# Kernel tuning notes

Measured on AMD Instinct MI355X. Metric: run time of the kernel, lower is better.

The kernel has to match this reference:

```python
import jax, jax.numpy as jnp
import numpy as np

BSZ = 2          # batch
H_IMG = 180      # BEV height
W_IMG = 180      # BEV width
BLK = 15         # block_size
D = 128          # d_model
NH = 8           # nhead
DH = D // NH     # head dim


def _bn_relu(x, g, b, m, v, eps=1e-5):
    # eval-mode BatchNorm2d followed by ReLU; x is NCHW
    s = g * jax.lax.rsqrt(v + eps)
    return jax.nn.relu((x - m[None, :, None, None]) * s[None, :, None, None]
                       + b[None, :, None, None])


def _split_tokens(x):
    # (B,C,H,W) -> (B*nb, blk*blk, C), block order = (row-block, col-block)
    B, C, H, W = x.shape
    hb, wb = H // BLK, W // BLK
    x = x.reshape(B, C, hb, BLK, wb, BLK)
    x = x.transpose(0, 2, 4, 1, 3, 5)              # (B,hb,wb,C,blk,blk)
    x = x.reshape(B * hb * wb, C, BLK * BLK)
    return x.transpose(0, 2, 1)                    # (B*nb, L, C)


def _merge_tokens(t, B, H, W):
    # (B*nb, L, C) -> (B,C,H,W), inverse of _split_tokens
    hb, wb = H // BLK, W // BLK
    C = t.shape[-1]
    x = t.transpose(0, 2, 1).reshape(B, hb, wb, C, BLK, BLK)
    x = x.transpose(0, 3, 1, 4, 2, 5)              # (B,C,hb,blk,wb,blk)
    return x.reshape(B, C, H, W)


def setup_inputs() -> dict:
    key = jax.random.key(0)
    ks = jax.random.split(key, 16)
    n = lambda i, shp, sc=0.05: jax.random.normal(ks[i], shp, jnp.float32) * sc
    inp = {
        'camera_feat': jax.random.normal(ks[0], (BSZ, 80, H_IMG, W_IMG), jnp.float32),
        'lidar_feat': jax.random.normal(ks[1], (BSZ, 256, H_IMG, W_IMG), jnp.float32),
        'cam_w': n(2, (D, 80)),
        'cam_gamma': jnp.ones((D,), jnp.float32),
        'cam_beta': jnp.zeros((D,), jnp.float32),
        'cam_mean': n(3, (D,)),
        'cam_var': jax.random.uniform(ks[4], (D,), jnp.float32, 0.5, 1.5),
        'lidar_w': n(5, (D, 256)),
        'lidar_gamma': jnp.ones((D,), jnp.float32),
        'lidar_beta': jnp.zeros((D,), jnp.float32),
        'lidar_mean': n(6, (D,)),
        'lidar_var': jax.random.uniform(ks[7], (D,), jnp.float32, 0.5, 1.5),
        'in_proj_w': n(8, (3 * D, D)),
        'in_proj_b': jnp.zeros((3 * D,), jnp.float32),
        'out_proj_w': n(9, (D, D)),
        'out_proj_b': jnp.zeros((D,), jnp.float32),
        'outc_w': n(10, (256, D, 3, 3)),
        'outc_gamma': jnp.ones((256,), jnp.float32),
        'outc_beta': jnp.zeros((256,), jnp.float32),
        'outc_mean': n(11, (256,)),
        'outc_var': jax.random.uniform(ks[12], (256,), jnp.float32, 0.5, 1.5),
    }
    return inp


def reference(camera_feat, lidar_feat,
              cam_w, cam_gamma, cam_beta, cam_mean, cam_var,
              lidar_w, lidar_gamma, lidar_beta, lidar_mean, lidar_var,
              in_proj_w, in_proj_b, out_proj_w, out_proj_b,
              outc_w, outc_gamma, outc_beta, outc_mean, outc_var):
    B, _, H, W = camera_feat.shape
    # 1x1 conv projections + BN + ReLU
    cam_p = _bn_relu(jnp.einsum('bchw,dc->bdhw', camera_feat, cam_w),
                     cam_gamma, cam_beta, cam_mean, cam_var)
    lid_p = _bn_relu(jnp.einsum('bchw,dc->bdhw', lidar_feat, lidar_w),
                     lidar_gamma, lidar_beta, lidar_mean, lidar_var)
    # windowed tokens: (B*nb, L=225, D)
    cam_t = _split_tokens(cam_p)
    lid_t = _split_tokens(lid_p)
    # cross-attention: query=lidar, key/value=camera (torch MHA math)
    wq, wk, wv = in_proj_w[:D], in_proj_w[D:2 * D], in_proj_w[2 * D:]
    bq, bk, bv = in_proj_b[:D], in_proj_b[D:2 * D], in_proj_b[2 * D:]
    BN, L, _ = lid_t.shape
    q = (lid_t @ wq.T + bq).reshape(BN, L, NH, DH).transpose(0, 2, 1, 3)
    k = (cam_t @ wk.T + bk).reshape(BN, L, NH, DH).transpose(0, 2, 1, 3)
    v = (cam_t @ wv.T + bv).reshape(BN, L, NH, DH).transpose(0, 2, 1, 3)
    scores = jnp.einsum('bhqd,bhkd->bhqk', q, k) / jnp.sqrt(jnp.float32(DH))
    attn = jax.nn.softmax(scores, axis=-1)
    ctx = jnp.einsum('bhqk,bhkd->bhqd', attn, v)
    ctx = ctx.transpose(0, 2, 1, 3).reshape(BN, L, D)
    attn_out = ctx @ out_proj_w.T + out_proj_b
    # merge windows back and fuse
    fused = _merge_tokens(attn_out, B, H, W) + lid_p
    # 3x3 conv + BN + ReLU
    y = jax.lax.conv_general_dilated(
        fused, outc_w, window_strides=(1, 1), padding='SAME',
        dimension_numbers=('NCHW', 'OIHW', 'NCHW'))
    return _bn_relu(y, outc_gamma, outc_beta, outc_mean, outc_var)
```

## Files before the change

### kernel.cpp

```cpp
#include <hip/hip_runtime.h>
#include <hip/hip_bf16.h>
#include <cmath>

#define HW      32400
#define WIMG    180
#define DD      128
#define NHEADS  8
#define DHEAD   16
#define LTOK    225
#define PSTRIDE 64928
#define FBROW   188
#define FBH     182
#define FBSZ    ((size_t)FBH * FBROW * 128)

typedef __attribute__((ext_vector_type(8))) short bf16x8;
typedef __attribute__((ext_vector_type(4))) float f32x4;

union U16B { uint4 u; int4 i; bf16x8 v; };

__device__ __forceinline__ bf16x8 ldfrag(const __hip_bfloat16* p, int ld, int lane) {
  return *(const bf16x8*)(p + (size_t)(lane & 15) * ld + ((lane >> 4) << 3));
}

__device__ __forceinline__ float bf2f(unsigned int u) {
  return __uint_as_float(u << 16);
}

__device__ __forceinline__ unsigned short f2bf(float x) {
  unsigned int b = __float_as_uint(x);
  return (unsigned short)((b + 0x7fffu + ((b >> 16) & 1u)) >> 16);
}

__global__ void k_cast(const float* __restrict__ in, __hip_bfloat16* __restrict__ out, int n) {
  int i = blockIdx.x * 256 + threadIdx.x;
  if (i < n) out[i] = __float2bfloat16(in[i]);
}

__global__ void k_prepproj(const float* __restrict__ w, __hip_bfloat16* __restrict__ wb,
                           int C, int Kpad) {
  int i = blockIdx.x * 256 + threadIdx.x;
  if (i >= 128 * Kpad) return;
  int d = i / Kpad, c = i % Kpad;
  wb[i] = (c < C) ? __float2bfloat16(w[d * C + c]) : __float2bfloat16(0.f);
}

__global__ void k_prepw2(const float* __restrict__ cw, __hip_bfloat16* __restrict__ wcb) {
  int i = blockIdx.x * 256 + threadIdx.x;
  if (i >= 294912) return;
  int oc16  = i / 18432;
  int r0    = i % 18432;
  int tap   = r0 / 2048;
  int r1    = r0 % 2048;
  int chunk = r1 / 512;
  int r2    = r1 % 512;
  int lane  = r2 / 8;
  int e     = r2 % 8;
  int oc = oc16 * 16 + (lane & 15);
  int ic = chunk * 32 + (lane >> 4) * 8 + e;
  wcb[i] = __float2bfloat16(cw[(size_t)(oc * 128 + ic) * 9 + tap]);
}

__global__ void k_zero(uint4* __restrict__ p, int n16) {
  int i = blockIdx.x * 256 + threadIdx.x;
  if (i < n16) p[i] = make_uint4(0u, 0u, 0u, 0u);
}

__global__ void __launch_bounds__(256) k_proj_mfma(
    const float* __restrict__ in, const __hip_bfloat16* __restrict__ wb,
    const float* __restrict__ g, const float* __restrict__ be,
    const float* __restrict__ mu, const float* __restrict__ var,
    __hip_bfloat16* __restrict__ outp, int C, int Kpad) {
  __shared__ __align__(16) __hip_bfloat16 sa[128 * 64];
  int m0 = blockIdx.x * 128;
  int b = blockIdx.z;
  int tid = threadIdx.x, lane = tid & 63, wid = tid >> 6;
  int wm = (wid >> 1) * 64, wn = (wid & 1) * 64;
  const float* inb = in + (size_t)b * C * HW;
  int sp = (tid >> 1) & 127;
  int sc4 = (tid & 1) * 4;
  int gp = m0 + sp;
  bool pok = gp < HW;
  f32x4 acc[4][4] = {};
  for (int kc = 0; kc < Kpad; kc += 64) {
    __syncthreads();
#pragma unroll
    for (int it = 0; it < 8; ++it) {
      int lc = sc4 + it * 8;
      int c = kc + lc;
      unsigned short u[4];
#pragma unroll
      for (int j = 0; j < 4; ++j) {
        float x = (pok && (c + j) < C) ? inb[(size_t)(c + j) * HW + gp] : 0.f;
        u[j] = f2bf(x);
      }
      int blk = (lc >> 3) ^ (sp & 7);
      char* dst = (char*)sa + sp * 128 + blk * 16 + (lc & 7) * 2;
      *(uint2*)dst = make_uint2(((unsigned)u[1] << 16) | u[0],
                                ((unsigned)u[3] << 16) | u[2]);
    }
    __syncthreads();
#pragma unroll
    for (int ks = 0; ks < 2; ++ks) {
      bf16x8 af[4], bfr[4];
#pragma unroll
      for (int i = 0; i < 4; ++i) {
        int pr = wm + i * 16 + (lane & 15);
        int blk = ((ks * 4 + (lane >> 4)) ^ (pr & 7));
        af[i] = *(const bf16x8*)((const char*)sa + pr * 128 + blk * 16);
      }
#pragma unroll
      for (int j = 0; j < 4; ++j)
        bfr[j] = ldfrag(wb + (size_t)(wn + j * 16) * Kpad + kc + ks * 32, Kpad, lane);
#pragma unroll
      for (int i = 0; i < 4; ++i)
#pragma unroll
        for (int j = 0; j < 4; ++j)
          acc[i][j] = __builtin_amdgcn_mfma_f32_16x16x32_bf16(af[i], bfr[j], acc[i][j], 0, 0, 0);
    }
  }
  int col = lane & 15, rq = lane >> 4;
  __hip_bfloat16* ob = outp + (size_t)b * PSTRIDE * 128;
#pragma unroll
  for (int j = 0; j < 4; ++j) {
    int d = wn + j * 16 + col;
    float s = g[d] * rsqrtf(var[d] + 1e-5f);
    float mm = mu[d], bb = be[d];
#pragma unroll
    for (int i = 0; i < 4; ++i) {
#pragma unroll
      for (int r = 0; r < 4; ++r) {
        int m = m0 + wm + i * 16 + rq * 4 + r;
        if (m < HW) {
          float y = (acc[i][j][r] - mm) * s + bb;
          ob[(size_t)m * 128 + d] = __float2bfloat16(fmaxf(y, 0.f));
        }
      }
    }
  }
}

__global__ void __launch_bounds__(256) k_gemm_bias(
    const __hip_bfloat16* __restrict__ A, const __hip_bfloat16* __restrict__ B,
    const float* __restrict__ bias, __hip_bfloat16* __restrict__ out,
    int K, int ldout) {
  int m0 = blockIdx.x * 128, n0 = blockIdx.y * 128, b = blockIdx.z;
  int lane = threadIdx.x & 63, wid = threadIdx.x >> 6;
  int wm = (wid >> 1) * 64, wn = (wid & 1) * 64;
  const __hip_bfloat16* Ab = A + (size_t)b * PSTRIDE * K;
  f32x4 acc[4][4] = {};
  for (int kc = 0; kc < K; kc += 32) {
    bf16x8 af[4], bfr[4];
#pragma unroll
    for (int i = 0; i < 4; ++i)
      af[i] = ldfrag(Ab + (size_t)(m0 + wm + i * 16) * K + kc, K, lane);
#pragma unroll
    for (int j = 0; j < 4; ++j)
      bfr[j] = ldfrag(B + (size_t)(n0 + wn + j * 16) * K + kc, K, lane);
#pragma unroll
    for (int i = 0; i < 4; ++i)
#pragma unroll
      for (int j = 0; j < 4; ++j)
        acc[i][j] = __builtin_amdgcn_mfma_f32_16x16x32_bf16(af[i], bfr[j], acc[i][j], 0, 0, 0);
  }
  int col = lane & 15, rq = lane >> 4;
  __hip_bfloat16* ob = out + (size_t)b * PSTRIDE * ldout;
#pragma unroll
  for (int j = 0; j < 4; ++j) {
    int n = n0 + wn + j * 16 + col;
    float bs = bias[n];
#pragma unroll
    for (int i = 0; i < 4; ++i) {
#pragma unroll
      for (int r = 0; r < 4; ++r) {
        int m = m0 + wm + i * 16 + rq * 4 + r;
        if (m < HW) ob[(size_t)m * ldout + n] = __float2bfloat16(acc[i][j][r] + bs);
      }
    }
  }
}

__global__ void __launch_bounds__(256) k_attn_mfma(
    const __hip_bfloat16* __restrict__ qc, const __hip_bfloat16* __restrict__ kvb,
    __hip_bfloat16* __restrict__ ctx) {
  __shared__ __align__(16) unsigned short ksh[240 * 32];
  __shared__ __align__(16) unsigned short vsh[16 * 248];
  __shared__ __align__(16) unsigned short psh[4 * 256];
  int bn = blockIdx.x, hh = blockIdx.y;
  int b = bn / 144, rr = bn % 144, tby = rr / 12, tbx = rr % 12;
  int tid = threadIdx.x;
  int pbase = tby * 15 * WIMG + tbx * 15;
  const __hip_bfloat16* kvbase = kvb + (size_t)b * PSTRIDE * 256 + hh * 16;

  if (tid < 240) {
    int row = tid;
    unsigned short kv16[16];
#pragma unroll
    for (int j = 0; j < 16; ++j) kv16[j] = 0;
    unsigned short vv16[16];
#pragma unroll
    for (int j = 0; j < 16; ++j) vv16[j] = 0;
    if (row < LTOK) {
      int p = pbase + (row / 15) * WIMG + (row % 15);
      const uint4* kp = (const uint4*)(kvbase + (size_t)p * 256);
      uint4 k0 = kp[0], k1 = kp[1];
      uint4 v0 = kp[16], v1 = kp[17];
      unsigned kw[8] = {k0.x, k0.y, k0.z, k0.w, k1.x, k1.y, k1.z, k1.w};
      unsigned vw[8] = {v0.x, v0.y, v0.z, v0.w, v1.x, v1.y, v1.z, v1.w};
#pragma unroll
      for (int j = 0; j < 8; ++j) {
        kv16[2 * j]     = (unsigned short)(__float_as_uint(bf2f(kw[j] & 0xffffu) * 0.25f) >> 16);
        kv16[2 * j + 1] = (unsigned short)(__float_as_uint(bf2f(kw[j] >> 16) * 0.25f) >> 16);
        vv16[2 * j]     = (unsigned short)(vw[j] & 0xffffu);
        vv16[2 * j + 1] = (unsigned short)(vw[j] >> 16);
      }
    }
    char* kbase = (char*)ksh + row * 64;
    uint4 zz = make_uint4(0, 0, 0, 0);
    *(uint4*)(kbase + ((0 ^ (row & 3)) << 4)) = ((uint4*)kv16)[0];
    *(uint4*)(kbase + ((1 ^ (row & 3)) << 4)) = ((uint4*)kv16)[1];
    *(uint4*)(kbase + ((2 ^ (row & 3)) << 4)) = zz;
    *(uint4*)(kbase + ((3 ^ (row & 3)) << 4)) = zz;
#pragma unroll
    for (int d = 0; d < 16; ++d) vsh[d * 248 + row] = vv16[d];
  }
  __syncthreads();

  int lane = tid & 63, wid = tid >> 6;
  int g = lane >> 4, q15 = lane & 15;
  int wq0 = wid * 64;
  char* pw_base = (char*)psh + wid * 512;

  bf16x8 qf[4];
#pragma unroll
  for (int i = 0; i < 4; ++i) {
    int q = wq0 + i * 16 + q15;
    int qq = q < LTOK ? q : 0;
    int p = pbase + (qq / 15) * WIMG + (qq % 15);
    U16B u; u.u = make_uint4(0, 0, 0, 0);
    if (g < 2) u.u = *(const uint4*)(qc + ((size_t)b * PSTRIDE + p) * 128 + hh * 16 + g * 8);
    qf[i] = u.v;
  }

  float m_[4], ls[4];
  f32x4 oac[4] = {};
#pragma unroll
  for (int i = 0; i < 4; ++i) { m_[i] = -3.0e38f; ls[i] = 0.f; }
  const f32x4 zacc = {};

  for (int ck = 0; ck < 15; ++ck) {
    int rowb = ck * 16 + q15;
    bf16x8 kf = *(const bf16x8*)((const char*)ksh + rowb * 64 + ((g ^ (rowb & 3)) << 4));
    U16B vu; vu.u = make_uint4(0, 0, 0, 0);
    if (g < 2) vu.u = *(const uint4*)((const char*)vsh + (q15 * 248 + ck * 16 + g * 8) * 2);
    bf16x8 vf = vu.v;
#pragma unroll
    for (int i = 0; i < 4; ++i) {
      f32x4 st = __builtin_amdgcn_mfma_f32_16x16x32_bf16(kf, qf[i], zacc, 0, 0, 0);
      float s0 = st[0], s1 = st[1], s2 = st[2], s3 = st[3];
      if (ck == 14) {
        s0 = (g == 0) ? s0 : -3.0e38f;
        s1 = -3.0e38f; s2 = -3.0e38f; s3 = -3.0e38f;
      }
      float cm = fmaxf(fmaxf(s0, s1), fmaxf(s2, s3));
      cm = fmaxf(cm, __shfl_xor(cm, 16));
      cm = fmaxf(cm, __shfl_xor(cm, 32));
      float mn = fmaxf(m_[i], cm);
      float corr = __expf(m_[i] - mn);
      float p0 = __expf(s0 - mn), p1 = __expf(s1 - mn);
      float p2 = __expf(s2 - mn), p3 = __expf(s3 - mn);
      float ps = (p0 + p1) + (p2 + p3);
      ps += __shfl_xor(ps, 16);
      ps += __shfl_xor(ps, 32);
      ls[i] = ls[i] * corr + ps;
      m_[i] = mn;
      unsigned w0 = (unsigned)f2bf(p0) | ((unsigned)f2bf(p1) << 16);
      unsigned w1 = (unsigned)f2bf(p2) | ((unsigned)f2bf(p3) << 16);
      *(uint2*)(pw_base + q15 * 32 + g * 8) = make_uint2(w0, w1);
      U16B pu; pu.u = make_uint4(0, 0, 0, 0);
      if (g < 2) pu.u = *(const uint4*)(pw_base + q15 * 32 + g * 16);
      f32x4 oc = oac[i];
      oc[0] *= corr; oc[1] *= corr; oc[2] *= corr; oc[3] *= corr;
      oac[i] = __builtin_amdgcn_mfma_f32_16x16x32_bf16(vf, pu.v, oc, 0, 0, 0);
    }
  }

  __hip_bfloat16* cb = ctx + (size_t)b * PSTRIDE * 128 + hh * 16;
#pragma unroll
  for (int i = 0; i < 4; ++i) {
    float inv = 1.f / ls[i];
    int qo = wq0 + i * 16 + q15;
    if (qo < LTOK) {
      unsigned lo = (unsigned)f2bf(oac[i][0] * inv) | ((unsigned)f2bf(oac[i][1] * inv) << 16);
      unsigned hi = (unsigned)f2bf(oac[i][2] * inv) | ((unsigned)f2bf(oac[i][3] * inv) << 16);
      int p = pbase + (qo / 15) * WIMG + (qo % 15);
      *(uint2*)(cb + (size_t)p * 128 + g * 4) = make_uint2(lo, hi);
    }
  }
}

__global__ void __launch_bounds__(256) k_outproj_mfma(
    const __hip_bfloat16* __restrict__ ctx, const __hip_bfloat16* __restrict__ wob,
    const float* __restrict__ opb, const __hip_bfloat16* __restrict__ lidb,
    __hip_bfloat16* __restrict__ fb) {
  int m0 = blockIdx.x * 128, b = blockIdx.z;
  int lane = threadIdx.x & 63, wid = threadIdx.x >> 6;
  int wm = (wid >> 1) * 64, wn = (wid & 1) * 64;
  const __hip_bfloat16* Ab = ctx + (size_t)b * PSTRIDE * 128;
  f32x4 acc[4][4] = {};
  for (int kc = 0; kc < 128; kc += 32) {
    bf16x8 af[4], bfr[4];
#pragma unroll
    for (int i = 0; i < 4; ++i)
      af[i] = ldfrag(Ab + (size_t)(m0 + wm + i * 16) * 128 + kc, 128, lane);
#pragma unroll
    for (int j = 0; j < 4; ++j)
      bfr[j] = ldfrag(wob + (size_t)(wn + j * 16) * 128 + kc, 128, lane);
#pragma unroll
    for (int i = 0; i < 4; ++i)
#pragma unroll
      for (int j = 0; j < 4; ++j)
        acc[i][j] = __builtin_amdgcn_mfma_f32_16x16x32_bf16(af[i], bfr[j], acc[i][j], 0, 0, 0);
  }
  int col = lane & 15, rq = lane >> 4;
  const __hip_bfloat16* lb = lidb + (size_t)b * PSTRIDE * 128;
  __hip_bfloat16* fbp = fb + (size_t)b * FBSZ;
#pragma unroll
  for (int j = 0; j < 4; ++j) {
    int n = wn + j * 16 + col;
    float bs = opb[n];
#pragma unroll
    for (int i = 0; i < 4; ++i) {
#pragma unroll
      for (int r = 0; r < 4; ++r) {
        int m = m0 + wm + i * 16 + rq * 4 + r;
        if (m < HW) {
          float v = acc[i][j][r] + bs + __bfloat162float(lb[(size_t)m * 128 + n]);
          int hhh = m / WIMG, www = m % WIMG;
          fbp[((size_t)(hhh + 1) * FBROW + (www + 1)) * 128 + n] = __float2bfloat16(v);
        }
      }
    }
  }
}

__global__ void __launch_bounds__(256) k_conv_mfma(
    const __hip_bfloat16* __restrict__ fb, const __hip_bfloat16* __restrict__ wcb,
    const float* __restrict__ g, const float* __restrict__ be,
    const float* __restrict__ mu, const float* __restrict__ var,
    float* __restrict__ out) {
  __shared__ __align__(16) uint4 Asm[2976];
  int bx = blockIdx.x;
  int h = bx / 6, rem = bx % 6;
  int strip = rem >> 1, ocg = rem & 1;
  int w0 = strip * 60;
  int b = blockIdx.z;
  int tid = threadIdx.x, lane = tid & 63, wid = tid >> 6;
  int q15 = lane & 15, kg = lane >> 4;
  int wpx = (wid & 1) * 32;
  const __hip_bfloat16* fbb = fb + (size_t)b * FBSZ;
  const __hip_bfloat16* Bw = wcb + (size_t)(ocg * 8 + (wid >> 1) * 4) * 18432 + lane * 8;

#pragma unroll
  for (int it = 0; it < 12; ++it) {
    int slot = it * 256 + tid;
    if (slot < 2976) {
      int px = slot % 62;
      int rowk = slot / 62;
      int dy = rowk >> 4, kgrp = rowk & 15;
      Asm[slot] = *(const uint4*)(fbb + ((size_t)(h + dy) * FBROW + (w0 + px)) * 128 + kgrp * 8);
    }
  }

#define LOADB(dst, t)                                                          \
  {                                                                            \
    int tap_ = (t) >> 2, ch_ = (t) & 3;                                        \
    _Pragma("unroll") for (int j = 0; j < 4; ++j)                              \
        dst[j] = *(const bf16x8*)(Bw + (size_t)j * 18432 + tap_ * 2048 + ch_ * 512); \
  }

  bf16x8 bp0[4], bp1[4], bp2[4];
  LOADB(bp0, 0);
  LOADB(bp1, 1);
  LOADB(bp2, 2);
  __syncthreads();

  f32x4 acc[2][4] = {};

#define STEP(t, bp)                                                            \
  {                                                                            \
    int tap_ = (t) >> 2, ch_ = (t) & 3;                                        \
    int dy_ = tap_ / 3, dx_ = tap_ % 3;                                        \
    int rowk_ = (dy_ * 16 + ch_ * 4 + kg) * 62;                                \
    bf16x8 af[2];                                                              \
    _Pragma("unroll") for (int i = 0; i < 2; ++i)                              \
        af[i] = *(const bf16x8*)&Asm[rowk_ + wpx + i * 16 + q15 + dx_];        \
    _Pragma("unroll") for (int i = 0; i < 2; ++i)                              \
        _Pragma("unroll") for (int j = 0; j < 4; ++j)                          \
            acc[i][j] = __builtin_amdgcn_mfma_f32_16x16x32_bf16(af[i], bp[j], acc[i][j], 0, 0, 0); \
  }

#pragma unroll
  for (int t = 0; t < 36; t += 3) {
    STEP(t, bp0);
    if (t + 3 < 36) LOADB(bp0, t + 3);
    STEP(t + 1, bp1);
    if (t + 4 < 36) LOADB(bp1, t + 4);
    STEP(t + 2, bp2);
    if (t + 5 < 36) LOADB(bp2, t + 5);
  }
#undef STEP
#undef LOADB

  int ocbase = ocg * 128 + (wid >> 1) * 64;
#pragma unroll
  for (int j = 0; j < 4; ++j) {
    int oc = ocbase + j * 16 + q15;
    float s = g[oc] * rsqrtf(var[oc] + 1e-5f);
    float mm = mu[oc], bb = be[oc];
#pragma unroll
    for (int i = 0; i < 2; ++i) {
      int pxb = wpx + i * 16 + kg * 4;
      if (pxb < 60) {
        float4 o4;
        o4.x = fmaxf((acc[i][j][0] - mm) * s + bb, 0.f);
        o4.y = fmaxf((acc[i][j][1] - mm) * s + bb, 0.f);
        o4.z = fmaxf((acc[i][j][2] - mm) * s + bb, 0.f);
        o4.w = fmaxf((acc[i][j][3] - mm) * s + bb, 0.f);
        *(float4*)(&out[(size_t)(b * 256 + oc) * HW + h * WIMG + w0 + pxb]) = o4;
      }
    }
  }
}

extern "C" void kernel_launch(void* const* d_in, const int* in_sizes, int n_in,
                              void* d_out, int out_size, void* d_ws, size_t ws_size,
                              hipStream_t stream) {
  const float* camera = (const float*)d_in[0];
  const float* lidar  = (const float*)d_in[1];
  const float* cam_w  = (const float*)d_in[2];
  const float* cam_g  = (const float*)d_in[3];
  const float* cam_b  = (const float*)d_in[4];
  const float* cam_m  = (const float*)d_in[5];
  const float* cam_v  = (const float*)d_in[6];
  const float* lid_w  = (const float*)d_in[7];
  const float* lid_g  = (const float*)d_in[8];
  const float* lid_b  = (const float*)d_in[9];
  const float* lid_m  = (const float*)d_in[10];
  const float* lid_v  = (const float*)d_in[11];
  const float* ipw    = (const float*)d_in[12];
  const float* ipb    = (const float*)d_in[13];
  const float* opw    = (const float*)d_in[14];
  const float* opb    = (const float*)d_in[15];
  const float* ocw    = (const float*)d_in[16];
  const float* ocg    = (const float*)d_in[17];
  const float* ocb    = (const float*)d_in[18];
  const float* ocm    = (const float*)d_in[19];
  const float* ocv    = (const float*)d_in[20];

  __hip_bfloat16* ws = (__hip_bfloat16*)d_ws;
  const size_t NP = (size_t)2 * PSTRIDE * 128;
  __hip_bfloat16* cam_bf = ws;
  __hip_bfloat16* lid_bf = ws + NP;
  __hip_bfloat16* qc     = ws + 2 * NP;
  __hip_bfloat16* kvb    = ws + 3 * NP;
  __hip_bfloat16* wipb   = ws + 5 * NP;
  __hip_bfloat16* wob    = wipb + 384 * 128;
  __hip_bfloat16* wcb    = wob + 128 * 128;
  __hip_bfloat16* wcamb  = wcb + 256 * 9 * 128;
  __hip_bfloat16* wlidb  = wcamb + 128 * 128;
  __hip_bfloat16* fbbuf  = cam_bf;

  dim3 blk(256);
  hipLaunchKernelGGL(k_cast, dim3(192), blk, 0, stream, ipw, wipb, 384 * 128);
  hipLaunchKernelGGL(k_cast, dim3(64), blk, 0, stream, opw, wob, 128 * 128);
  hipLaunchKernelGGL(k_prepw2, dim3(1152), blk, 0, stream, ocw, wcb);
  hipLaunchKernelGGL(k_prepproj, dim3(64), blk, 0, stream, cam_w, wcamb, 80, 128);
  hipLaunchKernelGGL(k_prepproj, dim3(128), blk, 0, stream, lid_w, wlidb, 256, 256);
  dim3 gproj(254, 1, 2);
  hipLaunchKernelGGL(k_proj_mfma, gproj, blk, 0, stream,
                     camera, wcamb, cam_g, cam_b, cam_m, cam_v, cam_bf, 80, 128);
  hipLaunchKernelGGL(k_proj_mfma, gproj, blk, 0, stream,
                     lidar, wlidb, lid_g, lid_b, lid_m, lid_v, lid_bf, 256, 256);
  hipLaunchKernelGGL(k_gemm_bias, dim3(254, 1, 2), blk, 0, stream,
                     lid_bf, wipb, ipb, qc, 128, 128);
  hipLaunchKernelGGL(k_gemm_bias, dim3(254, 2, 2), blk, 0, stream,
                     cam_bf, wipb + 128 * 128, ipb + 128, kvb, 128, 256);
  hipLaunchKernelGGL(k_attn_mfma, dim3(288, 8), blk, 0, stream, qc, kvb, qc);
  int n16 = (int)((2 * FBSZ * 2) / 16);
  hipLaunchKernelGGL(k_zero, dim3((n16 + 255) / 256), blk, 0, stream, (uint4*)fbbuf, n16);
  hipLaunchKernelGGL(k_outproj_mfma, dim3(254, 1, 2), blk, 0, stream,
                     qc, wob, opb, lid_bf, fbbuf);
  hipLaunchKernelGGL(k_conv_mfma, dim3(1080, 1, 2), blk, 0, stream,
                     fbbuf, wcb, ocg, ocb, ocm, ocv, (float*)d_out);
}
```

Measured before the change: 310.1 us.

## Use two-pass exp2 softmax in attention, fold scale into Q, zero only border

Folds the 1/sqrt(dh)·log2(e) factor into the Q projection epilogue. The attention kernel now runs a max pass first and then an exp2 pass, which removes the online-softmax rescaling and the per-chunk shuffles. K and V are stored in shared memory in MFMA fragment order so each fragment is a single vector load, and the in-kernel K scaling is dropped. Only the padding border of the fused buffer is zeroed instead of the whole buffer. The cost is recomputing QK^T twice, and the change assumes the outproj kernel writes every interior pixel.

```diff
diff --git a/kernel.cpp b/kernel.cpp
--- a/kernel.cpp
+++ b/kernel.cpp
@@ -12,6 +12,7 @@
 #define FBROW   188
 #define FBH     182
 #define FBSZ    ((size_t)FBH * FBROW * 128)
+#define QSCALE  0.36067376022224085f
 
 typedef __attribute__((ext_vector_type(8))) short bf16x8;
 typedef __attribute__((ext_vector_type(4))) float f32x4;
@@ -60,9 +61,19 @@
   wcb[i] = __float2bfloat16(cw[(size_t)(oc * 128 + ic) * 9 + tap]);
 }
 
-__global__ void k_zero(uint4* __restrict__ p, int n16) {
-  int i = blockIdx.x * 256 + threadIdx.x;
-  if (i < n16) p[i] = make_uint4(0u, 0u, 0u, 0u);
+__global__ void k_zero_border(__hip_bfloat16* __restrict__ fbb) {
+  int idx = blockIdx.x * 256 + threadIdx.x;
+  if (idx >= 2 * 736 * 16) return;
+  int b = idx / (736 * 16);
+  int r = idx % (736 * 16);
+  int px = r >> 4, blk = r & 15;
+  int row, col;
+  if (px < 188)      { row = 0;            col = px; }
+  else if (px < 376) { row = 181;          col = px - 188; }
+  else if (px < 556) { row = px - 376 + 1; col = 0; }
+  else               { row = px - 556 + 1; col = 181; }
+  ((uint4*)(fbb + (size_t)b * FBSZ + ((size_t)row * FBROW + col) * 128))[blk] =
+      make_uint4(0u, 0u, 0u, 0u);
 }
 
 __global__ void __launch_bounds__(256) k_proj_mfma(
@@ -142,7 +153,7 @@
 __global__ void __launch_bounds__(256) k_gemm_bias(
     const __hip_bfloat16* __restrict__ A, const __hip_bfloat16* __restrict__ B,
     const float* __restrict__ bias, __hip_bfloat16* __restrict__ out,
-    int K, int ldout) {
+    int K, int ldout, float oscale) {
   int m0 = blockIdx.x * 128, n0 = blockIdx.y * 128, b = blockIdx.z;
   int lane = threadIdx.x & 63, wid = threadIdx.x >> 6;
   int wm = (wid >> 1) * 64, wn = (wid & 1) * 64;
@@ -173,7 +184,7 @@
 #pragma unroll
       for (int r = 0; r < 4; ++r) {
         int m = m0 + wm + i * 16 + rq * 4 + r;
-        if (m < HW) ob[(size_t)m * ldout + n] = __float2bfloat16(acc[i][j][r] + bs);
+        if (m < HW) ob[(size_t)m * ldout + n] = __float2bfloat16((acc[i][j][r] + bs) * oscale);
       }
     }
   }
@@ -182,8 +193,8 @@
 __global__ void __launch_bounds__(256) k_attn_mfma(
     const __hip_bfloat16* __restrict__ qc, const __hip_bfloat16* __restrict__ kvb,
     __hip_bfloat16* __restrict__ ctx) {
-  __shared__ __align__(16) unsigned short ksh[240 * 32];
-  __shared__ __align__(16) unsigned short vsh[16 * 248];
+  __shared__ __align__(16) uint4 Kf[15 * 64];
+  __shared__ __align__(16) uint4 Vf[15 * 64];
   __shared__ __align__(16) unsigned short psh[4 * 256];
   int bn = blockIdx.x, hh = blockIdx.y;
   int b = bn / 144, rr = bn % 144, tby = rr / 12, tbx = rr % 12;
@@ -193,35 +204,28 @@
 
   if (tid < 240) {
     int row = tid;
-    unsigned short kv16[16];
-#pragma unroll
-    for (int j = 0; j < 16; ++j) kv16[j] = 0;
-    unsigned short vv16[16];
-#pragma unroll
-    for (int j = 0; j < 16; ++j) vv16[j] = 0;
+    int ck = row >> 4, q = row & 15;
+    uint4 k0 = make_uint4(0, 0, 0, 0), k1 = k0, v0 = k0, v1 = k0;
     if (row < LTOK) {
       int p = pbase + (row / 15) * WIMG + (row % 15);
       const uint4* kp = (const uint4*)(kvbase + (size_t)p * 256);
-      uint4 k0 = kp[0], k1 = kp[1];
-      uint4 v0 = kp[16], v1 = kp[17];
-      unsigned kw[8] = {k0.x, k0.y, k0.z, k0.w, k1.x, k1.y, k1.z, k1.w};
-      unsigned vw[8] = {v0.x, v0.y, v0.z, v0.w, v1.x, v1.y, v1.z, v1.w};
-#pragma unroll
-      for (int j = 0; j < 8; ++j) {
-        kv16[2 * j]     = (unsigned short)(__float_as_uint(bf2f(kw[j] & 0xffffu) * 0.25f) >> 16);
-        kv16[2 * j + 1] = (unsigned short)(__float_as_uint(bf2f(kw[j] >> 16) * 0.25f) >> 16);
-        vv16[2 * j]     = (unsigned short)(vw[j] & 0xffffu);
-        vv16[2 * j + 1] = (unsigned short)(vw[j] >> 16);
-      }
-    }
-    char* kbase = (char*)ksh + row * 64;
+      k0 = kp[0]; k1 = kp[1];
+      v0 = kp[16]; v1 = kp[17];
+    }
     uint4 zz = make_uint4(0, 0, 0, 0);
-    *(uint4*)(kbase + ((0 ^ (row & 3)) << 4)) = ((uint4*)kv16)[0];
-    *(uint4*)(kbase + ((1 ^ (row & 3)) << 4)) = ((uint4*)kv16)[1];
-    *(uint4*)(kbase + ((2 ^ (row & 3)) << 4)) = zz;
-    *(uint4*)(kbase + ((3 ^ (row & 3)) << 4)) = zz;
-#pragma unroll
-    for (int d = 0; d < 16; ++d) vsh[d * 248 + row] = vv16[d];
+    Kf[ck * 64 + q]      = k0;
+    Kf[ck * 64 + 16 + q] = k1;
+    Kf[ck * 64 + 32 + q] = zz;
+    Kf[ck * 64 + 48 + q] = zz;
+    unsigned short vv[16];
+    *(uint4*)&vv[0] = v0;
+    *(uint4*)&vv[8] = v1;
+    int vg = q >> 3, vj = q & 7;
+#pragma unroll
+    for (int d = 0; d < 16; ++d)
+      ((unsigned short*)&Vf[ck * 64 + vg * 16 + d])[vj] = vv[d];
+    Vf[ck * 64 + 32 + q] = zz;
+    Vf[ck * 64 + 48 + q] = zz;
   }
   __syncthreads();
 
@@ -229,6 +233,8 @@
   int g = lane >> 4, q15 = lane & 15;
   int wq0 = wid * 64;
   char* pw_base = (char*)psh + wid * 512;
+  const bf16x8* KfB = (const bf16x8*)Kf + lane;
+  const bf16x8* VfB = (const bf16x8*)Vf + lane;
 
   bf16x8 qf[4];
 #pragma unroll
@@ -241,47 +247,58 @@
     qf[i] = u.v;
   }
 
-  float m_[4], ls[4];
-  f32x4 oac[4] = {};
-#pragma unroll
-  for (int i = 0; i < 4; ++i) { m_[i] = -3.0e38f; ls[i] = 0.f; }
   const f32x4 zacc = {};
-
+  float cm[4];
+#pragma unroll
+  for (int i = 0; i < 4; ++i) cm[i] = -3.0e38f;
+
+#pragma unroll
   for (int ck = 0; ck < 15; ++ck) {
-    int rowb = ck * 16 + q15;
-    bf16x8 kf = *(const bf16x8*)((const char*)ksh + rowb * 64 + ((g ^ (rowb & 3)) << 4));
-    U16B vu; vu.u = make_uint4(0, 0, 0, 0);
-    if (g < 2) vu.u = *(const uint4*)((const char*)vsh + (q15 * 248 + ck * 16 + g * 8) * 2);
-    bf16x8 vf = vu.v;
+    bf16x8 kf = KfB[ck * 64];
 #pragma unroll
     for (int i = 0; i < 4; ++i) {
       f32x4 st = __builtin_amdgcn_mfma_f32_16x16x32_bf16(kf, qf[i], zacc, 0, 0, 0);
-      float s0 = st[0], s1 = st[1], s2 = st[2], s3 = st[3];
+      cm[i] = fmaxf(cm[i], fmaxf(fmaxf(st[0], st[1]), fmaxf(st[2], st[3])));
+    }
+  }
+#pragma unroll
+  for (int i = 0; i < 4; ++i) {
+    cm[i] = fmaxf(cm[i], __shfl_xor(cm[i], 16));
+    cm[i] = fmaxf(cm[i], __shfl_xor(cm[i], 32));
+  }
+
+  float ls[4] = {0.f, 0.f, 0.f, 0.f};
+  f32x4 oac[4] = {};
+#pragma unroll
+  for (int ck = 0; ck < 15; ++ck) {
+    bf16x8 kf = KfB[ck * 64];
+    bf16x8 vf = VfB[ck * 64];
+#pragma unroll
+    for (int i = 0; i < 4; ++i) {
+      f32x4 st = __builtin_amdgcn_mfma_f32_16x16x32_bf16(kf, qf[i], zacc, 0, 0, 0);
+      float p0 = exp2f(st[0] - cm[i]);
+      float p1 = exp2f(st[1] - cm[i]);
+      float p2 = exp2f(st[2] - cm[i]);
+      float p3 = exp2f(st[3] - cm[i]);
       if (ck == 14) {
-        s0 = (g == 0) ? s0 : -3.0e38f;
-        s1 = -3.0e38f; s2 = -3.0e38f; s3 = -3.0e38f;
-      }
-      float cm = fmaxf(fmaxf(s0, s1), fmaxf(s2, s3));
-      cm = fmaxf(cm, __shfl_xor(cm, 16));
-      cm = fmaxf(cm, __shfl_xor(cm, 32));
-      float mn = fmaxf(m_[i], cm);
-      float corr = __expf(m_[i] - mn);
-      float p0 = __expf(s0 - mn), p1 = __expf(s1 - mn);
-      float p2 = __expf(s2 - mn), p3 = __expf(s3 - mn);
-      float ps = (p0 + p1) + (p2 + p3);
-      ps += __shfl_xor(ps, 16);
-      ps += __shfl_xor(ps, 32);
-      ls[i] = ls[i] * corr + ps;
-      m_[i] = mn;
-      unsigned w0 = (unsigned)f2bf(p0) | ((unsigned)f2bf(p1) << 16);
-      unsigned w1 = (unsigned)f2bf(p2) | ((unsigned)f2bf(p3) << 16);
+        if (g) p0 = 0.f;
+        p1 = 0.f; p2 = 0.f; p3 = 0.f;
+      }
+      ls[i] += (p0 + p1) + (p2 + p3);
+      unsigned w0 = (unsigned)__bfloat16_as_ushort(__float2bfloat16(p0)) |
+                    ((unsigned)__bfloat16_as_ushort(__float2bfloat16(p1)) << 16);
+      unsigned w1 = (unsigned)__bfloat16_as_ushort(__float2bfloat16(p2)) |
+                    ((unsigned)__bfloat16_as_ushort(__float2bfloat16(p3)) << 16);
       *(uint2*)(pw_base + q15 * 32 + g * 8) = make_uint2(w0, w1);
       U16B pu; pu.u = make_uint4(0, 0, 0, 0);
       if (g < 2) pu.u = *(const uint4*)(pw_base + q15 * 32 + g * 16);
-      f32x4 oc = oac[i];
-      oc[0] *= corr; oc[1] *= corr; oc[2] *= corr; oc[3] *= corr;
-      oac[i] = __builtin_amdgcn_mfma_f32_16x16x32_bf16(vf, pu.v, oc, 0, 0, 0);
-    }
+      oac[i] = __builtin_amdgcn_mfma_f32_16x16x32_bf16(vf, pu.v, oac[i], 0, 0, 0);
+    }
+  }
+#pragma unroll
+  for (int i = 0; i < 4; ++i) {
+    ls[i] += __shfl_xor(ls[i], 16);
+    ls[i] += __shfl_xor(ls[i], 32);
   }
 
   __hip_bfloat16* cb = ctx + (size_t)b * PSTRIDE * 128 + hh * 16;
@@ -482,12 +499,11 @@
   hipLaunchKernelGGL(k_proj_mfma, gproj, blk, 0, stream,
                      lidar, wlidb, lid_g, lid_b, lid_m, lid_v, lid_bf, 256, 256);
   hipLaunchKernelGGL(k_gemm_bias, dim3(254, 1, 2), blk, 0, stream,
-                     lid_bf, wipb, ipb, qc, 128, 128);
+                     lid_bf, wipb, ipb, qc, 128, 128, QSCALE);
   hipLaunchKernelGGL(k_gemm_bias, dim3(254, 2, 2), blk, 0, stream,
-                     cam_bf, wipb + 128 * 128, ipb + 128, kvb, 128, 256);
+                     cam_bf, wipb + 128 * 128, ipb + 128, kvb, 128, 256, 1.0f);
   hipLaunchKernelGGL(k_attn_mfma, dim3(288, 8), blk, 0, stream, qc, kvb, qc);
-  int n16 = (int)((2 * FBSZ * 2) / 16);
-  hipLaunchKernelGGL(k_zero, dim3((n16 + 255) / 256), blk, 0, stream, (uint4*)fbbuf, n16);
+  hipLaunchKernelGGL(k_zero_border, dim3(92), blk, 0, stream, fbbuf);
   hipLaunchKernelGGL(k_outproj_mfma, dim3(254, 1, 2), blk, 0, stream,
                      qc, wob, opb, lid_bf, fbbuf);
   hipLaunchKernelGGL(k_conv_mfma, dim3(1080, 1, 2), blk, 0, stream,
```

Measured after the change: 355.2 us. 14.5% more time.
